# Optimization experiments

Measured on AMD Instinct MI355X. Metric: run time of the kernel, lower is better.

## Reference

```python
import jax, jax.numpy as jnp
import numpy as np

TAU = 0.07          # temperature
NUM_CLASSES = 1000  # label vocabulary size (used for bincount length)


def setup_inputs() -> dict:
    key = jax.random.key(0)
    kq, kk, ky = jax.random.split(key, 3)
    N, K, D = 8192, 8, 512
    q = jax.random.normal(kq, (N, D), dtype=jnp.float32)
    q = q / jnp.linalg.norm(q, axis=1, keepdims=True)          # L2-normalized anchors
    k = jax.random.normal(kk, (N, K, D), dtype=jnp.float32)
    k = k / jnp.linalg.norm(k, axis=2, keepdims=True)          # L2-normalized positives
    y = jax.random.randint(ky, (N,), 0, NUM_CLASSES, dtype=jnp.int32)
    return {"q": q, "k": k, "y": y}


def reference(q, k, y):
    # q: [N, D] anchors, k: [N, K, D] external positives, y: [N] labels
    N, K, D = k.shape
    neg_inf = jnp.float32(-jnp.inf)

    # similarities to external positives and within-batch, scaled by temperature
    k_sims = jnp.einsum('nd,nkd->nk', q, k) / TAU            # [N, K]
    batch_sims = jnp.matmul(q, q.T) / TAU                    # [N, N]

    same = y[:, None] == y[None, :]                          # [N, N] label equality
    eye = jnp.eye(N, dtype=bool)
    same_class_mask = same & ~eye                            # in-batch positives (excl. self)
    same_class_counts = same_class_mask.sum(axis=1) + K      # [N]

    # faithful to torch: multiply by mask then masked_fill(x == 0, -inf)
    batch_pos = batch_sims * same_class_mask
    batch_pos = jnp.where(batch_pos == 0, neg_inf, batch_pos)
    pos_sims = jnp.concatenate([k_sims, batch_pos], axis=1)  # [N, K+N]
    num = jax.scipy.special.logsumexp(pos_sims, axis=1)      # [N]

    y_counts = jnp.bincount(y, length=NUM_CLASSES)           # [C]
    neg_sims = batch_sims * (~same)
    neg_sims = jnp.where(neg_sims == 0, neg_inf, neg_sims)
    # class-frequency-weighted denominator (as in the original, no max-shift)
    den = jnp.log(jnp.sum(jnp.exp(neg_sims) / y_counts[y][None, :].astype(q.dtype), axis=1))

    loss = -(num - den) / same_class_counts.astype(q.dtype)
    return loss.mean()
```

## Files before the change

### kernel.cpp

```cpp
#include <hip/hip_runtime.h>
#include <hip/hip_fp8.h>
#include <stdint.h>

constexpr int N    = 8192;
constexpr int D    = 512;
constexpr int KEXT = 8;
constexpr int NCLS = 1000;
#define TAU_INV  14.285714285714285714f
#define SC_L2    4.539816423767765f

typedef long   long2_t __attribute__((ext_vector_type(2)));
typedef float  f32x4   __attribute__((ext_vector_type(4)));
typedef int    v8i     __attribute__((ext_vector_type(8)));

typedef __attribute__((address_space(1))) void gvoid;
typedef __attribute__((address_space(3))) void lvoid;

__device__ __forceinline__ uint32_t pack4_e4m3(float a, float b, float c, float d) {
    __hip_fp8_e4m3 A(a), B(b), C(c), D(d);
    return (uint32_t)A.__x | ((uint32_t)B.__x << 8) |
           ((uint32_t)C.__x << 16) | ((uint32_t)D.__x << 24);
}

__device__ __forceinline__ f32x4 mfma128(long2_t alo, long2_t ahi,
                                         long2_t blo, long2_t bhi, f32x4 c) {
    union U { long2_t h[2]; v8i v; } A, B;
    A.h[0] = alo; A.h[1] = ahi;
    B.h[0] = blo; B.h[1] = bhi;
    return __builtin_amdgcn_mfma_scale_f32_16x16x128_f8f6f4(
        A.v, B.v, c, 0, 0, 0, 127, 0, 127);
}

__global__ void prep_k(const float* __restrict__ q, const int* __restrict__ y,
                       uint32_t* __restrict__ qf8, int* __restrict__ counts,
                       float* __restrict__ invy, float* __restrict__ pos,
                       float* __restrict__ neg) {
    const int b = blockIdx.x, tid = threadIdx.x;
    if (b == 0) {
        __shared__ int h[NCLS];
        for (int i = tid; i < NCLS; i += 256) h[i] = 0;
        __syncthreads();
        for (int i = tid; i < N; i += 256) atomicAdd(&h[y[i]], 1);
        __syncthreads();
        for (int i = tid; i < NCLS; i += 256) counts[i] = h[i];
        for (int i = tid; i < N; i += 256) invy[i] = 1.0f / (float)h[y[i]];
        return;
    }
    const int gid = (b - 1) * 256 + tid;
    const int row = gid >> 4;
    const int kb  = gid & 15;
    const int ks4 = kb >> 2, quad = kb & 3;
    const float* src = q + (size_t)row * D + kb * 32;
    uint32_t o[8];
#pragma unroll
    for (int j = 0; j < 8; j++) {
        float4 v = *reinterpret_cast<const float4*>(src + j * 4);
        o[j] = pack4_e4m3(v.x * SC_L2, v.y * SC_L2, v.z * SC_L2, v.w * SC_L2);
    }
    const int t = row >> 4, l15 = row & 15;
    const size_t s16 = (size_t)((t * 4 + ks4) * 128) + quad * 16 + l15;
    uint4* dst = reinterpret_cast<uint4*>(qf8);
    dst[s16]      = make_uint4(o[0], o[1], o[2], o[3]);
    dst[s16 + 64] = make_uint4(o[4], o[5], o[6], o[7]);
    if (gid < N) { pos[gid] = 0.f; neg[gid] = 0.f; }
}

__global__ __launch_bounds__(256, 2) void gemm_k(
        const uint32_t* __restrict__ qf8,
        const int* __restrict__ y,
        const float* __restrict__ invy,
        float* __restrict__ pos_sum,
        float* __restrict__ neg_sum) {
    __shared__ long2_t Asl[4096];
    __shared__ int   yRow[128];
    __shared__ float redP[2][128];
    __shared__ float redN[2][128];

    const int tid  = threadIdx.x;
    const int wave = tid >> 6;
    const int lane = tid & 63;
    const int quad = lane >> 4;
    const int l15  = lane & 15;

    const int ib     = blockIdx.x >> 3;
    const int jchunk = blockIdx.x & 7;
    const int ibase  = ib * 128;

    {
        const uint32_t* src = qf8 + (size_t)ib * 16384;
#pragma unroll
        for (int it = 0; it < 16; it++) {
            const int idx = it * 256 + tid;
            __builtin_amdgcn_global_load_lds((gvoid*)(src + idx * 4),
                                             (lvoid*)(Asl + idx), 16, 0, 0);
        }
    }
    if (tid < 128) {
        yRow[tid] = y[ibase + tid];
        redP[0][tid] = 0.f; redP[1][tid] = 0.f;
        redN[0][tid] = 0.f; redN[1][tid] = 0.f;
    }
    __syncthreads();

    const int wr = (wave >> 1) * 64;
    const int wc = (wave & 1) * 64;
    const int half = wave & 1;

    const long2_t* fbL = reinterpret_cast<const long2_t*>(qf8);
    const long2_t* pB[4];
#pragma unroll
    for (int m = 0; m < 4; m++)
        pB[m] = fbL + (size_t)(jchunk * 64 + (wc >> 4) + m) * 512 + lane;

    const int tA = wr >> 4;

    long2_t blo[2][4], bhi[2][4];
#pragma unroll
    for (int m = 0; m < 4; m++) {
        blo[0][m] = pB[m][0];
        bhi[0][m] = pB[m][64];
    }

    for (int jt = 0; jt < 8; jt++) {
        const int j0 = jchunk * 1024 + jt * 128;

        int   yjv[4];
        float icj[4];
#pragma unroll
        for (int mj = 0; mj < 4; mj++) {
            int jc = j0 + wc + mj * 16 + l15;
            yjv[mj] = y[jc];
            icj[mj] = invy[jc];
        }

        f32x4 acc[4][4];
#pragma unroll
        for (int a = 0; a < 4; a++)
#pragma unroll
            for (int c = 0; c < 4; c++) acc[a][c] = (f32x4)0.0f;

#pragma unroll
        for (int ks4 = 0; ks4 < 4; ks4++) {
            const int cur = ks4 & 1, nxt = cur ^ 1;
            if (ks4 < 3) {
#pragma unroll
                for (int m = 0; m < 4; m++) {
                    blo[nxt][m] = pB[m][(ks4 + 1) * 128];
                    bhi[nxt][m] = pB[m][(ks4 + 1) * 128 + 64];
                }
            } else if (jt < 7) {
#pragma unroll
                for (int m = 0; m < 4; m++) {
                    blo[nxt][m] = pB[m][4096];
                    bhi[nxt][m] = pB[m][4096 + 64];
                }
            }
            long2_t alo[4], ahi[4];
#pragma unroll
            for (int m = 0; m < 4; m++) {
                alo[m] = Asl[((tA + m) * 4 + ks4) * 128 + lane];
                ahi[m] = Asl[((tA + m) * 4 + ks4) * 128 + 64 + lane];
            }
#pragma unroll
            for (int mi = 0; mi < 4; mi++)
#pragma unroll
                for (int mj = 0; mj < 4; mj++)
                    acc[mi][mj] = mfma128(alo[mi], ahi[mi],
                                          blo[cur][mj], bhi[cur][mj],
                                          acc[mi][mj]);
        }
#pragma unroll
        for (int m = 0; m < 4; m++) pB[m] += 4096;

#pragma unroll
        for (int mi = 0; mi < 4; mi++) {
#pragma unroll
            for (int r = 0; r < 4; r++) {
                const int il   = wr + mi * 16 + quad * 4 + r;
                const int irow = ibase + il;
                const int myi  = yRow[il];
                float ps = 0.f, ns = 0.f;
#pragma unroll
                for (int mj = 0; mj < 4; mj++) {
                    const int jcol = j0 + wc + mj * 16 + l15;
                    float a    = acc[mi][mj][r];
                    float ex   = __builtin_amdgcn_exp2f(a);
                    bool  nz   = (a != 0.0f);
                    bool  same = (myi == yjv[mj]);
                    ps += (same && (irow != jcol) && nz) ? ex : 0.0f;
                    ns += (!same && nz) ? ex * icj[mj] : 0.0f;
                }
#pragma unroll
                for (int off = 1; off < 16; off <<= 1) {
                    ps += __shfl_xor(ps, off);
                    ns += __shfl_xor(ns, off);
                }
                if (l15 == 0) {
                    redP[half][il] += ps;
                    redN[half][il] += ns;
                }
            }
        }
    }

    __syncthreads();
    if (tid < 128) {
        atomicAdd(&pos_sum[ibase + tid], redP[0][tid] + redP[1][tid]);
    } else if (tid < 256) {
        const int il = tid - 128;
        atomicAdd(&neg_sum[ibase + il], redN[0][il] + redN[1][il]);
    }
}

__global__ void finalize_k(const float* __restrict__ q, const float* __restrict__ kmat,
                           const int* __restrict__ y, const int* __restrict__ counts,
                           const float* __restrict__ pos_sum, const float* __restrict__ neg_sum,
                           float* __restrict__ loss) {
    const int wave = threadIdx.x >> 6, lane = threadIdx.x & 63;
    const int i = blockIdx.x * 4 + wave;

    const float4* q4 = reinterpret_cast<const float4*>(q) + (size_t)i * 128;
    const float4* k4 = reinterpret_cast<const float4*>(kmat) + (size_t)i * KEXT * 128;
    float4 qa = q4[lane], qb = q4[lane + 64];

    float esum = 0.f;
    for (int kk = 0; kk < KEXT; kk++) {
        float4 ka = k4[(size_t)kk * 128 + lane];
        float4 kb = k4[(size_t)kk * 128 + lane + 64];
        float p = qa.x * ka.x;
        p = fmaf(qa.y, ka.y, p); p = fmaf(qa.z, ka.z, p); p = fmaf(qa.w, ka.w, p);
        p = fmaf(qb.x, kb.x, p); p = fmaf(qb.y, kb.y, p);
        p = fmaf(qb.z, kb.z, p); p = fmaf(qb.w, kb.w, p);
#pragma unroll
        for (int off = 1; off < 64; off <<= 1) p += __shfl_xor(p, off);
        esum += __expf(p * TAU_INV);
    }
    if (lane == 0) {
        float num = logf(esum + pos_sum[i]);
        float den = logf(neg_sum[i]);
        float cnt = (float)(counts[y[i]] - 1 + KEXT);
        loss[i] = -(num - den) / cnt;
    }
}

__global__ void reduce_k(const float* __restrict__ loss, float* __restrict__ out) {
    __shared__ float part[16];
    int tid = threadIdx.x;
    float s = 0.f;
    for (int i = tid; i < N; i += 1024) s += loss[i];
#pragma unroll
    for (int off = 1; off < 64; off <<= 1) s += __shfl_xor(s, off);
    if ((tid & 63) == 0) part[tid >> 6] = s;
    __syncthreads();
    if (tid < 16) {
        float v = part[tid];
#pragma unroll
        for (int off = 1; off < 16; off <<= 1) v += __shfl_xor(v, off);
        if (tid == 0) out[0] = v / (float)N;
    }
}

extern "C" void kernel_launch(void* const* d_in, const int* in_sizes, int n_in,
                              void* d_out, int out_size, void* d_ws, size_t ws_size,
                              hipStream_t stream) {
    const float* q    = (const float*)d_in[0];
    const float* kmat = (const float*)d_in[1];
    const int*   y    = (const int*)d_in[2];
    float* out = (float*)d_out;

    char* ws = (char*)d_ws;
    uint32_t* qf8  = (uint32_t*)ws;
    int*   counts  = (int*)  (ws + 4194304);
    float* invy    = (float*)(ws + 4198400);
    float* pos     = (float*)(ws + 4231168);
    float* neg     = (float*)(ws + 4263936);
    float* loss    = (float*)(ws + 4296704);

    prep_k    <<<1 + (N * 16) / 256, 256, 0, stream>>>(q, y, qf8, counts, invy, pos, neg);
    gemm_k    <<<512, 256, 0, stream>>>(qf8, y, invy, pos, neg);
    finalize_k<<<N / 4, 256, 0, stream>>>(q, kmat, y, counts, pos, neg, loss);
    reduce_k  <<<1, 1024, 0, stream>>>(loss, out);
}
```

Measured before the change: 355.6 us.

## Switch FP8 GEMM to 32x32x64 MFMA and defer row reductions to end

Replaces the 16x16x128 scaled FP8 MFMA with the 32x32x64 variant, which requires a new packed layout for q in the prep kernel and new fragment indexing in the GEMM. Per-row partial sums are now kept in registers across all column tiles, and the cross-lane shuffle reduction and LDS writes happen once at the end instead of after every tile. The aim is fewer MFMA issues and fewer fragment loads per FLOP, plus less shuffle and LDS traffic. The cost is higher register pressure (32-float accumulators plus 64 partial-sum registers), which may hurt occupancy under the launch bounds of 2 blocks per SIMD.

```diff
diff --git a/kernel.cpp b/kernel.cpp
--- a/kernel.cpp
+++ b/kernel.cpp
@@ -10,7 +10,7 @@
 #define SC_L2    4.539816423767765f
 
 typedef long   long2_t __attribute__((ext_vector_type(2)));
-typedef float  f32x4   __attribute__((ext_vector_type(4)));
+typedef float  f32x16  __attribute__((ext_vector_type(16)));
 typedef int    v8i     __attribute__((ext_vector_type(8)));
 
 typedef __attribute__((address_space(1))) void gvoid;
@@ -22,12 +22,12 @@
            ((uint32_t)C.__x << 16) | ((uint32_t)D.__x << 24);
 }
 
-__device__ __forceinline__ f32x4 mfma128(long2_t alo, long2_t ahi,
-                                         long2_t blo, long2_t bhi, f32x4 c) {
+__device__ __forceinline__ f32x16 mfma32(long2_t alo, long2_t ahi,
+                                         long2_t blo, long2_t bhi, f32x16 c) {
     union U { long2_t h[2]; v8i v; } A, B;
     A.h[0] = alo; A.h[1] = ahi;
     B.h[0] = blo; B.h[1] = bhi;
-    return __builtin_amdgcn_mfma_scale_f32_16x16x128_f8f6f4(
+    return __builtin_amdgcn_mfma_scale_f32_32x32x64_f8f6f4(
         A.v, B.v, c, 0, 0, 0, 127, 0, 127);
 }
 
@@ -46,20 +46,20 @@
         for (int i = tid; i < N; i += 256) invy[i] = 1.0f / (float)h[y[i]];
         return;
     }
-    const int gid = (b - 1) * 256 + tid;
-    const int row = gid >> 4;
-    const int kb  = gid & 15;
-    const int ks4 = kb >> 2, quad = kb & 3;
-    const float* src = q + (size_t)row * D + kb * 32;
+    const int gid  = (b - 1) * 256 + tid;
+    const int grp  = gid >> 6;
+    const int lane = gid & 63;
+    const int row  = (grp >> 3) * 32 + (lane & 31);
+    const int k0   = (grp & 7) * 64 + (lane >> 5) * 32;
+    const float* src = q + (size_t)row * D + k0;
     uint32_t o[8];
 #pragma unroll
     for (int j = 0; j < 8; j++) {
         float4 v = *reinterpret_cast<const float4*>(src + j * 4);
         o[j] = pack4_e4m3(v.x * SC_L2, v.y * SC_L2, v.z * SC_L2, v.w * SC_L2);
     }
-    const int t = row >> 4, l15 = row & 15;
-    const size_t s16 = (size_t)((t * 4 + ks4) * 128) + quad * 16 + l15;
     uint4* dst = reinterpret_cast<uint4*>(qf8);
+    const size_t s16 = (size_t)grp * 128 + lane;
     dst[s16]      = make_uint4(o[0], o[1], o[2], o[3]);
     dst[s16 + 64] = make_uint4(o[4], o[5], o[6], o[7]);
     if (gid < N) { pos[gid] = 0.f; neg[gid] = 0.f; }
@@ -72,15 +72,15 @@
         float* __restrict__ pos_sum,
         float* __restrict__ neg_sum) {
     __shared__ long2_t Asl[4096];
-    __shared__ int   yRow[128];
+    __shared__ int   yR[128];
     __shared__ float redP[2][128];
     __shared__ float redN[2][128];
 
     const int tid  = threadIdx.x;
     const int wave = tid >> 6;
     const int lane = tid & 63;
-    const int quad = lane >> 4;
-    const int l15  = lane & 15;
+    const int l31  = lane & 31;
+    const int hi   = lane >> 5;
 
     const int ib     = blockIdx.x >> 3;
     const int jchunk = blockIdx.x & 7;
@@ -95,28 +95,38 @@
                                              (lvoid*)(Asl + idx), 16, 0, 0);
         }
     }
-    if (tid < 128) {
-        yRow[tid] = y[ibase + tid];
-        redP[0][tid] = 0.f; redP[1][tid] = 0.f;
-        redN[0][tid] = 0.f; redN[1][tid] = 0.f;
-    }
+    if (tid < 128) yR[tid] = y[ibase + tid];
     __syncthreads();
 
-    const int wr = (wave >> 1) * 64;
-    const int wc = (wave & 1) * 64;
-    const int half = wave & 1;
+    const int wr   = (wave >> 1) * 64;
+    const int wc   = (wave & 1) * 64;
+    const int colh = wave & 1;
+    const int tA   = wr >> 5;
+
+    uint32_t yiP[16];
+#pragma unroll
+    for (int mi = 0; mi < 2; mi++)
+#pragma unroll
+        for (int rr = 0; rr < 8; rr++) {
+            const int r0 = 2 * rr, r1 = 2 * rr + 1;
+            const int il0 = wr + mi * 32 + (r0 & 3) + 8 * (r0 >> 2) + 4 * hi;
+            const int il1 = wr + mi * 32 + (r1 & 3) + 8 * (r1 >> 2) + 4 * hi;
+            yiP[mi * 8 + rr] = (uint32_t)yR[il0] | ((uint32_t)yR[il1] << 16);
+        }
+
+    float posp[32], negp[32];
+#pragma unroll
+    for (int e = 0; e < 32; e++) { posp[e] = 0.f; negp[e] = 0.f; }
 
     const long2_t* fbL = reinterpret_cast<const long2_t*>(qf8);
-    const long2_t* pB[4];
-#pragma unroll
-    for (int m = 0; m < 4; m++)
-        pB[m] = fbL + (size_t)(jchunk * 64 + (wc >> 4) + m) * 512 + lane;
-
-    const int tA = wr >> 4;
-
-    long2_t blo[2][4], bhi[2][4];
-#pragma unroll
-    for (int m = 0; m < 4; m++) {
+    const long2_t* pB[2];
+#pragma unroll
+    for (int m = 0; m < 2; m++)
+        pB[m] = fbL + (size_t)(jchunk * 32 + (wc >> 5) + m) * 1024 + lane;
+
+    long2_t blo[2][2], bhi[2][2];
+#pragma unroll
+    for (int m = 0; m < 2; m++) {
         blo[0][m] = pB[m][0];
         bhi[0][m] = pB[m][64];
     }
@@ -124,65 +134,66 @@
     for (int jt = 0; jt < 8; jt++) {
         const int j0 = jchunk * 1024 + jt * 128;
 
-        int   yjv[4];
-        float icj[4];
-#pragma unroll
-        for (int mj = 0; mj < 4; mj++) {
-            int jc = j0 + wc + mj * 16 + l15;
+        int   yjv[2];
+        float icj[2];
+#pragma unroll
+        for (int mj = 0; mj < 2; mj++) {
+            const int jc = j0 + wc + mj * 32 + l31;
             yjv[mj] = y[jc];
             icj[mj] = invy[jc];
         }
 
-        f32x4 acc[4][4];
-#pragma unroll
-        for (int a = 0; a < 4; a++)
-#pragma unroll
-            for (int c = 0; c < 4; c++) acc[a][c] = (f32x4)0.0f;
-
-#pragma unroll
-        for (int ks4 = 0; ks4 < 4; ks4++) {
-            const int cur = ks4 & 1, nxt = cur ^ 1;
-            if (ks4 < 3) {
-#pragma unroll
-                for (int m = 0; m < 4; m++) {
-                    blo[nxt][m] = pB[m][(ks4 + 1) * 128];
-                    bhi[nxt][m] = pB[m][(ks4 + 1) * 128 + 64];
+        f32x16 acc[2][2];
+#pragma unroll
+        for (int a = 0; a < 2; a++)
+#pragma unroll
+            for (int c = 0; c < 2; c++) acc[a][c] = (f32x16)0.0f;
+
+#pragma unroll
+        for (int ks2 = 0; ks2 < 8; ks2++) {
+            const int cur = ks2 & 1, nxt = cur ^ 1;
+            if (ks2 < 7) {
+#pragma unroll
+                for (int m = 0; m < 2; m++) {
+                    blo[nxt][m] = pB[m][(ks2 + 1) * 128];
+                    bhi[nxt][m] = pB[m][(ks2 + 1) * 128 + 64];
                 }
             } else if (jt < 7) {
 #pragma unroll
-                for (int m = 0; m < 4; m++) {
+                for (int m = 0; m < 2; m++) {
                     blo[nxt][m] = pB[m][4096];
                     bhi[nxt][m] = pB[m][4096 + 64];
                 }
             }
-            long2_t alo[4], ahi[4];
-#pragma unroll
-            for (int m = 0; m < 4; m++) {
-                alo[m] = Asl[((tA + m) * 4 + ks4) * 128 + lane];
-                ahi[m] = Asl[((tA + m) * 4 + ks4) * 128 + 64 + lane];
-            }
-#pragma unroll
-            for (int mi = 0; mi < 4; mi++)
-#pragma unroll
-                for (int mj = 0; mj < 4; mj++)
-                    acc[mi][mj] = mfma128(alo[mi], ahi[mi],
-                                          blo[cur][mj], bhi[cur][mj],
-                                          acc[mi][mj]);
-        }
-#pragma unroll
-        for (int m = 0; m < 4; m++) pB[m] += 4096;
-
-#pragma unroll
-        for (int mi = 0; mi < 4; mi++) {
-#pragma unroll
-            for (int r = 0; r < 4; r++) {
-                const int il   = wr + mi * 16 + quad * 4 + r;
+            long2_t alo[2], ahi[2];
+#pragma unroll
+            for (int m = 0; m < 2; m++) {
+                alo[m] = Asl[((tA + m) * 8 + ks2) * 128 + lane];
+                ahi[m] = Asl[((tA + m) * 8 + ks2) * 128 + 64 + lane];
+            }
+#pragma unroll
+            for (int mi = 0; mi < 2; mi++)
+#pragma unroll
+                for (int mj = 0; mj < 2; mj++)
+                    acc[mi][mj] = mfma32(alo[mi], ahi[mi],
+                                         blo[cur][mj], bhi[cur][mj],
+                                         acc[mi][mj]);
+        }
+#pragma unroll
+        for (int m = 0; m < 2; m++) pB[m] += 4096;
+
+#pragma unroll
+        for (int mi = 0; mi < 2; mi++) {
+#pragma unroll
+            for (int r = 0; r < 16; r++) {
+                const int il   = wr + mi * 32 + (r & 3) + 8 * (r >> 2) + 4 * hi;
                 const int irow = ibase + il;
-                const int myi  = yRow[il];
+                const uint32_t p = yiP[mi * 8 + (r >> 1)];
+                const int myi = (int)((r & 1) ? (p >> 16) : (p & 0xffffu));
                 float ps = 0.f, ns = 0.f;
 #pragma unroll
-                for (int mj = 0; mj < 4; mj++) {
-                    const int jcol = j0 + wc + mj * 16 + l15;
+                for (int mj = 0; mj < 2; mj++) {
+                    const int jcol = j0 + wc + mj * 32 + l31;
                     float a    = acc[mi][mj][r];
                     float ex   = __builtin_amdgcn_exp2f(a);
                     bool  nz   = (a != 0.0f);
@@ -190,19 +201,29 @@
                     ps += (same && (irow != jcol) && nz) ? ex : 0.0f;
                     ns += (!same && nz) ? ex * icj[mj] : 0.0f;
                 }
-#pragma unroll
-                for (int off = 1; off < 16; off <<= 1) {
-                    ps += __shfl_xor(ps, off);
-                    ns += __shfl_xor(ns, off);
-                }
-                if (l15 == 0) {
-                    redP[half][il] += ps;
-                    redN[half][il] += ns;
-                }
-            }
-        }
-    }
-
+                posp[mi * 16 + r] += ps;
+                negp[mi * 16 + r] += ns;
+            }
+        }
+    }
+
+#pragma unroll
+    for (int mi = 0; mi < 2; mi++) {
+#pragma unroll
+        for (int r = 0; r < 16; r++) {
+            float ps = posp[mi * 16 + r], ns = negp[mi * 16 + r];
+#pragma unroll
+            for (int off = 1; off < 32; off <<= 1) {
+                ps += __shfl_xor(ps, off);
+                ns += __shfl_xor(ns, off);
+            }
+            if (l31 == 0) {
+                const int il = wr + mi * 32 + (r & 3) + 8 * (r >> 2) + 4 * hi;
+                redP[colh][il] = ps;
+                redN[colh][il] = ns;
+            }
+        }
+    }
     __syncthreads();
     if (tid < 128) {
         atomicAdd(&pos_sum[ibase + tid], redP[0][tid] + redP[1][tid]);
```

After: 395.1 us. +11.1%, slower.
